# Kernel tuning notes

Hardware: AMD Instinct MI355X
Metric: run time of the kernel (lower is better)

## Reference

```python
import jax, jax.numpy as jnp
import numpy as np

EPS = 1e-5

def _ste(x, q):
    # straight-through estimator: forward=q, backward=identity
    return x + jax.lax.stop_gradient(q - x)

def act_quant(x):
    # per-token int8 absmax quantization (BitNet b1.58 style), fake-quantized
    scale = 127.0 / jnp.clip(jnp.max(jnp.abs(x), axis=-1, keepdims=True), EPS)
    q = jnp.clip(jnp.round(x * scale), -128.0, 127.0) / scale
    return _ste(x, q)

def weight_quant(w):
    # ternary {-1,0,1} weights scaled by mean absolute value
    s = jnp.clip(jnp.mean(jnp.abs(w)), EPS)
    q = jnp.clip(jnp.round(w / s), -1.0, 1.0) * s
    return _ste(w, q)

def bit_linear(x, w):
    # x: [..., in], w: [out, in]
    return jnp.einsum('bsi,oi->bso', act_quant(x), weight_quant(w))

def setup_inputs() -> dict:
    key = jax.random.key(0)
    k1, k2, k3 = jax.random.split(key, 3)
    d_model, hidden = 2048, 4 * 2048
    x = jax.random.normal(k1, (4, 2048, d_model), dtype=jnp.float32)
    w1 = jax.random.normal(k2, (hidden, d_model), dtype=jnp.float32) * 0.02
    w2 = jax.random.normal(k3, (d_model, hidden), dtype=jnp.float32) * 0.02
    return {"x": x, "w1": w1, "w2": w2}

def reference(x, w1, w2):
    h = bit_linear(x, w1)            # [B, S, 4*d]
    h = jax.nn.gelu(h, approximate=False)  # exact erf GELU (nn.GELU default)
    return bit_linear(h, w2)         # [B, S, d]
```

## Files before the change

kernel.cpp:

```cpp
#include <hip/hip_runtime.h>
#include <hip/hip_bf16.h>
#include <hip/hip_fp16.h>
#include <stdint.h>

#define TPB 256
#define EPSF 1e-5f

using i32x4 = __attribute__((ext_vector_type(4))) int;


__device__ __forceinline__ void gload16(const void* g, void* l) {
    __builtin_amdgcn_global_load_lds(
        (__attribute__((address_space(1))) void*)g,
        (__attribute__((address_space(3))) void*)l,
        16, 0, 0);
}

__device__ __forceinline__ float wave_reduce_sum(float v) {
#pragma unroll
    for (int off = 32; off > 0; off >>= 1) v += __shfl_down(v, off, 64);
    return v;
}

__device__ __forceinline__ float wave_reduce_max(float v) {
#pragma unroll
    for (int off = 32; off > 0; off >>= 1) v = fmaxf(v, __shfl_down(v, off, 64));
    return v;
}

__device__ __forceinline__ int q8(float f, float scale, float lo, float hi) {
    return (int)fminf(fmaxf(rintf(f * scale), lo), hi);
}


__global__ void abssum_partial(const float* __restrict__ w, int n4,
                               float* __restrict__ part) {
    const float4* w4 = (const float4*)w;
    float acc = 0.f;
    for (int i = blockIdx.x * TPB + threadIdx.x; i < n4; i += gridDim.x * TPB) {
        float4 v = w4[i];
        acc += fabsf(v.x) + fabsf(v.y) + fabsf(v.z) + fabsf(v.w);
    }
    acc = wave_reduce_sum(acc);
    __shared__ float sh[4];
    if ((threadIdx.x & 63) == 0) sh[threadIdx.x >> 6] = acc;
    __syncthreads();
    if (threadIdx.x == 0) part[blockIdx.x] = sh[0] + sh[1] + sh[2] + sh[3];
}

__global__ void finalize_scales(const float* __restrict__ part1,
                                const float* __restrict__ part2,
                                float* __restrict__ scales, int nparts, float inv_n) {
    float a = 0.f, b = 0.f;
    for (int i = threadIdx.x; i < nparts; i += TPB) { a += part1[i]; b += part2[i]; }
    a = wave_reduce_sum(a);
    b = wave_reduce_sum(b);
    __shared__ float sa[4], sb[4];
    if ((threadIdx.x & 63) == 0) { sa[threadIdx.x >> 6] = a; sb[threadIdx.x >> 6] = b; }
    __syncthreads();
    if (threadIdx.x == 0) {
        scales[0] = fmaxf((sa[0] + sa[1] + sa[2] + sa[3]) * inv_n, EPSF);
        scales[1] = fmaxf((sb[0] + sb[1] + sb[2] + sb[3]) * inv_n, EPSF);
    }
}


__global__ void quant_w_i8(const float* __restrict__ w,
                           signed char* __restrict__ wq,
                           const float* __restrict__ scales, int sidx, int n4) {
    const float inv = 1.0f / scales[sidx];
    const float4* w4 = (const float4*)w;
    unsigned* oq = (unsigned*)wq;
    for (int i = blockIdx.x * TPB + threadIdx.x; i < n4; i += gridDim.x * TPB) {
        float4 v = w4[i];
        unsigned p = ((unsigned)(q8(v.x, inv, -1.f, 1.f) & 0xff)) |
                     ((unsigned)(q8(v.y, inv, -1.f, 1.f) & 0xff) << 8) |
                     ((unsigned)(q8(v.z, inv, -1.f, 1.f) & 0xff) << 16) |
                     ((unsigned)(q8(v.w, inv, -1.f, 1.f) & 0xff) << 24);
        oq[i] = p;
    }
}


template <int NF4>
__global__ void quant_x_i8(const float* __restrict__ in,
                           signed char* __restrict__ outq,
                           float* __restrict__ dq, int cols) {
    const long long row = blockIdx.x;
    const float4* r4 = (const float4*)(in + row * (long long)cols);
    float4 v[NF4];
    float mx = 0.f;
#pragma unroll
    for (int j = 0; j < NF4; ++j) {
        v[j] = r4[threadIdx.x + TPB * j];
        mx = fmaxf(mx, fmaxf(fmaxf(fabsf(v[j].x), fabsf(v[j].y)),
                             fmaxf(fabsf(v[j].z), fabsf(v[j].w))));
    }
    mx = wave_reduce_max(mx);
    __shared__ float sh[4];
    __shared__ float res;
    if ((threadIdx.x & 63) == 0) sh[threadIdx.x >> 6] = mx;
    __syncthreads();
    if (threadIdx.x == 0) res = fmaxf(fmaxf(sh[0], sh[1]), fmaxf(sh[2], sh[3]));
    __syncthreads();
    const float clipped = fmaxf(res, EPSF);
    const float scale = 127.f / clipped;
    if (threadIdx.x == 0) dq[row] = clipped / 127.f;
    unsigned* oq = (unsigned*)(outq + row * (long long)cols);
#pragma unroll
    for (int j = 0; j < NF4; ++j) {
        unsigned p = ((unsigned)(q8(v[j].x, scale, -128.f, 127.f) & 0xff)) |
                     ((unsigned)(q8(v[j].y, scale, -128.f, 127.f) & 0xff) << 8) |
                     ((unsigned)(q8(v[j].z, scale, -128.f, 127.f) & 0xff) << 16) |
                     ((unsigned)(q8(v[j].w, scale, -128.f, 127.f) & 0xff) << 24);
        oq[threadIdx.x + TPB * j] = p;
    }
}


template <int NJ>
__global__ void quant_h_i8(const unsigned short* __restrict__ h,
                           signed char* __restrict__ outq,
                           float* __restrict__ dq, int cols) {
    const long long row = blockIdx.x;
    const unsigned short* rp = h + row * (long long)cols;
    uint4 v[NJ];
    float mx = 0.f;
#pragma unroll
    for (int j = 0; j < NJ; ++j) {
        v[j] = *(const uint4*)(rp + (threadIdx.x + TPB * j) * 8);
        const unsigned* u = (const unsigned*)&v[j];
#pragma unroll
        for (int e = 0; e < 4; ++e) {
            float2 f2 = __half22float2(*(const __half2*)&u[e]);
            mx = fmaxf(mx, fmaxf(fabsf(f2.x), fabsf(f2.y)));
        }
    }
    mx = wave_reduce_max(mx);
    __shared__ float sh[4];
    __shared__ float res;
    if ((threadIdx.x & 63) == 0) sh[threadIdx.x >> 6] = mx;
    __syncthreads();
    if (threadIdx.x == 0) res = fmaxf(fmaxf(sh[0], sh[1]), fmaxf(sh[2], sh[3]));
    __syncthreads();
    const float clipped = fmaxf(res, EPSF);
    const float scale = 127.f / clipped;
    if (threadIdx.x == 0) dq[row] = clipped / 127.f;
    uint2* oq = (uint2*)(outq + row * (long long)cols);
#pragma unroll
    for (int j = 0; j < NJ; ++j) {
        const unsigned* u = (const unsigned*)&v[j];
        unsigned o[2] = {0, 0};
#pragma unroll
        for (int e = 0; e < 4; ++e) {
            float2 f2 = __half22float2(*(const __half2*)&u[e]);
            unsigned b0 = (unsigned)(q8(f2.x, scale, -128.f, 127.f) & 0xff);
            unsigned b1 = (unsigned)(q8(f2.y, scale, -128.f, 127.f) & 0xff);
            o[e >> 1] |= (b0 | (b1 << 8)) << ((e & 1) * 16);
        }
        oq[threadIdx.x + TPB * j] = *(uint2*)o;
    }
}


__device__ __forceinline__ void stage_half(const char* Xb, long long rowB, int prow,
                                           int tk, char* dst, int tid, int cbs) {
    const long long gc = (long long)tk * 128 + cbs;
    const int r = tid >> 3;
    gload16(Xb + (long long)(prow + r) * rowB + gc, dst + tid * 16);
    gload16(Xb + (long long)(prow + 64 + r) * rowB + gc, dst + 8192 + tid * 16);
}

#define QUAD(MB, NB)                                                            \
    _Pragma("unroll") for (int mi = 0; mi < 4; ++mi)                            \
    _Pragma("unroll") for (int ni = 0; ni < 2; ++ni)                            \
    _Pragma("unroll") for (int ks = 0; ks < 2; ++ks)                            \
        acc[(MB)*4 + mi][(NB)*2 + ni] = __builtin_amdgcn_mfma_i32_16x16x64_i8(  \
            aq[mi][ks], bq[(NB)*2 + ni][ks], acc[(MB)*4 + mi][(NB)*2 + ni], 0, 0, 0);

template <int OUT>
__global__ __launch_bounds__(512, 2) void gemm8p_i8(
    const signed char* __restrict__ A, const signed char* __restrict__ B,
    void* __restrict__ Cv, int N, int K,
    const float* __restrict__ dq, const float* __restrict__ scales, int sidx) {
    __shared__ __align__(16) char lds[131072];

    const int tid = threadIdx.x;
    const int lane = tid & 63;
    const int wid = tid >> 6;
    const int wr = wid >> 2;
    const int wc = wid & 3;

    const unsigned gx = gridDim.x;
    unsigned lin = blockIdx.y * gx + blockIdx.x;
    const unsigned qq = (gx * gridDim.y) >> 3;
    lin = (lin & 7) * qq + (lin >> 3);
    const unsigned bx = lin % gx;
    const unsigned by = lin / gx;

    const long long M0 = (long long)by * 256;
    const long long N0 = (long long)bx * 256;
    const long long rb = (long long)K;
    const char* Ab = (const char*)A + M0 * rb;
    const char* Bb = (const char*)B + N0 * rb;
    const int nt = K >> 7;

    const int cbs = (((tid & 7) ^ ((tid >> 3) & 7)) << 4);

    const int l15 = lane & 15, l4 = lane >> 4;
    const int swz = (lane & 7) << 4;
    const int acb0 = (l4 * 16) ^ swz;
    const int acb1 = (64 + l4 * 16) ^ swz;
    const int aoff = wr * 16384;
    const int boff = 32768 + (wc >> 1) * 16384 + (wc & 1) * 8192;

    i32x4 acc[8][4] = {};
    i32x4 aq[4][2], bq[4][2];

    stage_half(Bb, rb, 0,   0, lds + 32768,         tid, cbs);
    stage_half(Bb, rb, 128, 0, lds + 32768 + 16384, tid, cbs);
    stage_half(Ab, rb, 0,   0, lds + 0,             tid, cbs);
    stage_half(Ab, rb, 128, 0, lds + 16384,         tid, cbs);
    if (nt > 1) {
        stage_half(Bb, rb, 0,   1, lds + 65536 + 32768,         tid, cbs);
        stage_half(Bb, rb, 128, 1, lds + 65536 + 32768 + 16384, tid, cbs);
        stage_half(Ab, rb, 0,   1, lds + 65536,                 tid, cbs);
        asm volatile("s_waitcnt vmcnt(6)" ::: "memory");
    } else {
        asm volatile("s_waitcnt vmcnt(0)" ::: "memory");
    }
    __builtin_amdgcn_sched_barrier(0);
    __builtin_amdgcn_s_barrier();

    for (int t = 0; t < nt; ++t) {
        char* cur = lds + ((t & 1) << 16);
        char* nxt = lds + (((t + 1) & 1) << 16);
        const bool s1 = (t + 1) < nt;
        const bool s2 = (t + 2) < nt;

#pragma unroll
        for (int mi = 0; mi < 4; ++mi) {
            const char* p = cur + aoff + (mi * 16 + l15) * 128;
            aq[mi][0] = *(const i32x4*)(p + acb0);
            aq[mi][1] = *(const i32x4*)(p + acb1);
        }
#pragma unroll
        for (int ni = 0; ni < 4; ++ni) {
            const char* p = cur + boff + (ni * 16 + l15) * 128;
            bq[ni][0] = *(const i32x4*)(p + acb0);
            bq[ni][1] = *(const i32x4*)(p + acb1);
        }
        if (s1) stage_half(Ab, rb, 128, t + 1, nxt + 16384, tid, cbs);
        __builtin_amdgcn_s_setprio(1);
        QUAD(0, 0);
        __builtin_amdgcn_s_setprio(0);
        __builtin_amdgcn_s_barrier();

        if (s2) stage_half(Bb, rb, 0, t + 2, cur + 32768, tid, cbs);
        __builtin_amdgcn_s_setprio(1);
        QUAD(0, 1);
        __builtin_amdgcn_s_setprio(0);
        __builtin_amdgcn_s_barrier();

#pragma unroll
        for (int mi = 0; mi < 4; ++mi) {
            const char* p = cur + aoff + ((mi + 4) * 16 + l15) * 128;
            aq[mi][0] = *(const i32x4*)(p + acb0);
            aq[mi][1] = *(const i32x4*)(p + acb1);
        }
        if (s2) stage_half(Bb, rb, 128, t + 2, cur + 32768 + 16384, tid, cbs);
        __builtin_amdgcn_s_setprio(1);
        QUAD(1, 0);
        __builtin_amdgcn_s_setprio(0);
        __builtin_amdgcn_s_barrier();

        if (s2) stage_half(Ab, rb, 0, t + 2, cur, tid, cbs);
        __builtin_amdgcn_s_setprio(1);
        QUAD(1, 1);
        __builtin_amdgcn_s_setprio(0);
        if (s2) { asm volatile("s_waitcnt vmcnt(6)" ::: "memory"); }
        else    { asm volatile("s_waitcnt vmcnt(0)" ::: "memory"); }
        __builtin_amdgcn_sched_barrier(0);
        __builtin_amdgcn_s_barrier();
    }

    const float s = scales[sidx];
#pragma unroll
    for (int mi = 0; mi < 8; ++mi) {
#pragma unroll
        for (int r = 0; r < 4; ++r) {
            const long long m = M0 + wr * 128 + mi * 16 + l4 * 4 + r;
            const float f = dq[m] * s;
#pragma unroll
            for (int ni = 0; ni < 4; ++ni) {
                const long long n = N0 + wc * 64 + ni * 16 + l15;
                float v = (float)acc[mi][ni][r] * f;
                if (OUT) {
                    v = 0.5f * v * (1.0f + erff(v * 0.70710678118654752440f));
                    __half hh = __float2half(v);
                    __builtin_nontemporal_store(
                        *(const unsigned short*)&hh,
                        (unsigned short*)Cv + m * (long long)N + n);
                } else {
                    __builtin_nontemporal_store(
                        v, (float*)Cv + m * (long long)N + n);
                }
            }
        }
    }
}


extern "C" void kernel_launch(void* const* d_in, const int* in_sizes, int n_in,
                              void* d_out, int out_size, void* d_ws, size_t ws_size,
                              hipStream_t stream) {
    (void)n_in; (void)out_size;
    const float* x  = (const float*)d_in[0];
    const float* w1 = (const float*)d_in[1];
    const float* w2 = (const float*)d_in[2];
    float* out = (float*)d_out;

    const int D = 2048, H = 8192;
    const long long M = (long long)in_sizes[0] / D;

    char* base = (char*)d_ws;
    size_t off = 0;
    auto alloc = [&](size_t bytes) -> char* {
        char* r = base + off;
        off = (off + bytes + 255) & ~(size_t)255;
        return r;
    };

    const bool fullM = ws_size >= (size_t)236 * 1024 * 1024;
    const long long MC = fullM ? M : M / 2;

    float* part1 = (float*)alloc(2048 * 4);
    float* part2 = (float*)alloc(2048 * 4);
    float* scales = (float*)alloc(256);
    float* dqx = (float*)alloc((size_t)M * 4);
    float* dqh = (float*)alloc((size_t)M * 4);
    signed char* wq = (signed char*)alloc((size_t)H * D);
    signed char* xq = (signed char*)alloc((size_t)M * D);
    signed char* hq = (signed char*)alloc((size_t)M * H);
    unsigned short* hf = (unsigned short*)alloc((size_t)MC * H * 2);

    const int nw4 = H * D / 4;
    abssum_partial<<<2048, TPB, 0, stream>>>(w1, nw4, part1);
    abssum_partial<<<2048, TPB, 0, stream>>>(w2, nw4, part2);
    finalize_scales<<<1, TPB, 0, stream>>>(part1, part2, scales, 2048,
                                           1.0f / (float)(H * D));
    quant_w_i8<<<2048, TPB, 0, stream>>>(w1, wq, scales, 0, nw4);
    quant_x_i8<2><<<(int)M, TPB, 0, stream>>>(x, xq, dqx, D);

    if (fullM) {
        gemm8p_i8<1><<<dim3(H / 256, (int)(M / 256)), 512, 0, stream>>>(
            xq, wq, hf, H, D, dqx, scales, 0);
        quant_h_i8<4><<<(int)M, TPB, 0, stream>>>(hf, hq, dqh, H);
    } else {
        for (int g = 0; g < 2; ++g) {
            const long long m0 = g * MC;
            gemm8p_i8<1><<<dim3(H / 256, (int)(MC / 256)), 512, 0, stream>>>(
                xq + m0 * D, wq, hf, H, D, dqx + m0, scales, 0);
            quant_h_i8<4><<<(int)MC, TPB, 0, stream>>>(hf, hq + m0 * H, dqh + m0, H);
        }
    }

    quant_w_i8<<<2048, TPB, 0, stream>>>(w2, wq, scales, 1, nw4);

    gemm8p_i8<0><<<dim3(D / 256, (int)(M / 256)), 512, 0, stream>>>(
        hq, wq, out, D, H, dqh, scales, 1);
}
```

Baseline: 408.1 us.

## Switch int8 GEMM to 4-wave 256x128 tiles, fuse abssum, use tanh GELU

The int8 GEMM now runs 256-thread blocks of four waves on 256x128 output tiles instead of 512-thread 256x256 tiles, with a smaller 48KB LDS double buffer. It also changes the XCD-aware block remapping and adds explicit lgkmcnt waits before the MFMA blocks. The two weight abs-sum kernels are merged into one launch. Exact erf GELU is replaced with a tanh-style approximation built on exp2 and rcp, and the fp16 hidden store is no longer nontemporal. The GELU approximation changes numerics slightly, and the smaller tile re-reads the A operand more often in exchange for more blocks per CU.

```diff
diff --git a/kernel.cpp b/kernel.cpp
--- a/kernel.cpp
+++ b/kernel.cpp
@@ -32,12 +32,21 @@
     return (int)fminf(fmaxf(rintf(f * scale), lo), hi);
 }
 
-
-__global__ void abssum_partial(const float* __restrict__ w, int n4,
-                               float* __restrict__ part) {
-    const float4* w4 = (const float4*)w;
+__device__ __forceinline__ float gelu_fast(float x) {
+    float x2 = x * x;
+    float u = x * (0.7978845608f + 0.0356774081f * x2);
+    float e = exp2f(u * -2.8853900817779268f);
+    return x * __builtin_amdgcn_rcpf(1.0f + e);
+}
+
+
+__global__ void abssum2(const float* __restrict__ w1, const float* __restrict__ w2,
+                        int n4, float* __restrict__ part) {
+    const bool second = blockIdx.x >= 2048;
+    const float4* w4 = (const float4*)(second ? w2 : w1);
+    const int b = blockIdx.x & 2047;
     float acc = 0.f;
-    for (int i = blockIdx.x * TPB + threadIdx.x; i < n4; i += gridDim.x * TPB) {
+    for (int i = b * TPB + threadIdx.x; i < n4; i += 2048 * TPB) {
         float4 v = w4[i];
         acc += fabsf(v.x) + fabsf(v.y) + fabsf(v.z) + fabsf(v.w);
     }
@@ -48,11 +57,10 @@
     if (threadIdx.x == 0) part[blockIdx.x] = sh[0] + sh[1] + sh[2] + sh[3];
 }
 
-__global__ void finalize_scales(const float* __restrict__ part1,
-                                const float* __restrict__ part2,
-                                float* __restrict__ scales, int nparts, float inv_n) {
+__global__ void finalize_scales(const float* __restrict__ part,
+                                float* __restrict__ scales, float inv_n) {
     float a = 0.f, b = 0.f;
-    for (int i = threadIdx.x; i < nparts; i += TPB) { a += part1[i]; b += part2[i]; }
+    for (int i = threadIdx.x; i < 2048; i += TPB) { a += part[i]; b += part[i + 2048]; }
     a = wave_reduce_sum(a);
     b = wave_reduce_sum(b);
     __shared__ float sa[4], sb[4];
@@ -163,12 +171,15 @@
 }
 
 
-__device__ __forceinline__ void stage_half(const char* Xb, long long rowB, int prow,
-                                           int tk, char* dst, int tid, int cbs) {
+template <int N32>
+__device__ __forceinline__ void stageN(const char* Xb, long long rowB, int prow,
+                                       int tk, char* dst, int tid, int cbs) {
     const long long gc = (long long)tk * 128 + cbs;
     const int r = tid >> 3;
-    gload16(Xb + (long long)(prow + r) * rowB + gc, dst + tid * 16);
-    gload16(Xb + (long long)(prow + 64 + r) * rowB + gc, dst + 8192 + tid * 16);
+#pragma unroll
+    for (int j = 0; j < N32; ++j)
+        gload16(Xb + (long long)(prow + j * 32 + r) * rowB + gc,
+                dst + j * 4096 + tid * 16);
 }
 
 #define QUAD(MB, NB)                                                            \
@@ -178,54 +189,69 @@
         acc[(MB)*4 + mi][(NB)*2 + ni] = __builtin_amdgcn_mfma_i32_16x16x64_i8(  \
             aq[mi][ks], bq[(NB)*2 + ni][ks], acc[(MB)*4 + mi][(NB)*2 + ni], 0, 0, 0);
 
+#define READ_A(BUF, base_mi)                                                    \
+    _Pragma("unroll") for (int mi = 0; mi < 4; ++mi) {                          \
+        const char* p = (BUF) + aoff + ((mi + (base_mi)) * 16 + l15) * 128;     \
+        aq[mi][0] = *(const i32x4*)(p + acb0);                                  \
+        aq[mi][1] = *(const i32x4*)(p + acb1);                                  \
+    }
+#define READ_B(BUF)                                                             \
+    _Pragma("unroll") for (int ni = 0; ni < 4; ++ni) {                          \
+        const char* p = (BUF) + boff + (ni * 16 + l15) * 128;                   \
+        bq[ni][0] = *(const i32x4*)(p + acb0);                                  \
+        bq[ni][1] = *(const i32x4*)(p + acb1);                                  \
+    }
+
+#define LGKM0 do { asm volatile("s_waitcnt lgkmcnt(0)" ::: "memory");           \
+                   __builtin_amdgcn_sched_barrier(0); } while (0)
+
+#define BUFSZ 49152
+
 template <int OUT>
-__global__ __launch_bounds__(512, 2) void gemm8p_i8(
+__global__ __launch_bounds__(256, 2) void gemm4w(
     const signed char* __restrict__ A, const signed char* __restrict__ B,
     void* __restrict__ Cv, int N, int K,
     const float* __restrict__ dq, const float* __restrict__ scales, int sidx) {
-    __shared__ __align__(16) char lds[131072];
+    __shared__ __align__(16) char lds[2 * BUFSZ];
 
     const int tid = threadIdx.x;
     const int lane = tid & 63;
     const int wid = tid >> 6;
-    const int wr = wid >> 2;
-    const int wc = wid & 3;
+    const int wr = wid >> 1;
+    const int wc = wid & 1;
 
     const unsigned gx = gridDim.x;
-    unsigned lin = blockIdx.y * gx + blockIdx.x;
-    const unsigned qq = (gx * gridDim.y) >> 3;
-    lin = (lin & 7) * qq + (lin >> 3);
-    const unsigned bx = lin % gx;
-    const unsigned by = lin / gx;
+    const unsigned orig = blockIdx.y * gx + blockIdx.x;
+    const unsigned bpx = gx >> 3;
+    const unsigned xcd = orig & 7, jj = orig >> 3;
+    const unsigned bx = xcd * bpx + jj % bpx;
+    const unsigned by = jj / bpx;
 
     const long long M0 = (long long)by * 256;
-    const long long N0 = (long long)bx * 256;
+    const long long N0 = (long long)bx * 128;
     const long long rb = (long long)K;
     const char* Ab = (const char*)A + M0 * rb;
     const char* Bb = (const char*)B + N0 * rb;
     const int nt = K >> 7;
 
     const int cbs = (((tid & 7) ^ ((tid >> 3) & 7)) << 4);
-
     const int l15 = lane & 15, l4 = lane >> 4;
     const int swz = (lane & 7) << 4;
     const int acb0 = (l4 * 16) ^ swz;
     const int acb1 = (64 + l4 * 16) ^ swz;
     const int aoff = wr * 16384;
-    const int boff = 32768 + (wc >> 1) * 16384 + (wc & 1) * 8192;
+    const int boff = 32768 + wc * 8192;
 
     i32x4 acc[8][4] = {};
     i32x4 aq[4][2], bq[4][2];
 
-    stage_half(Bb, rb, 0,   0, lds + 32768,         tid, cbs);
-    stage_half(Bb, rb, 128, 0, lds + 32768 + 16384, tid, cbs);
-    stage_half(Ab, rb, 0,   0, lds + 0,             tid, cbs);
-    stage_half(Ab, rb, 128, 0, lds + 16384,         tid, cbs);
+    stageN<4>(Bb, rb, 0,   0, lds + 32768, tid, cbs);
+    stageN<4>(Ab, rb, 0,   0, lds + 0,     tid, cbs);
+    stageN<4>(Ab, rb, 128, 0, lds + 16384, tid, cbs);
     if (nt > 1) {
-        stage_half(Bb, rb, 0,   1, lds + 65536 + 32768,         tid, cbs);
-        stage_half(Bb, rb, 128, 1, lds + 65536 + 32768 + 16384, tid, cbs);
-        stage_half(Ab, rb, 0,   1, lds + 65536,                 tid, cbs);
-        asm volatile("s_waitcnt vmcnt(6)" ::: "memory");
+        stageN<4>(Bb, rb, 0, 1, lds + BUFSZ + 32768, tid, cbs);
+        stageN<4>(Ab, rb, 0, 1, lds + BUFSZ,         tid, cbs);
+        asm volatile("s_waitcnt vmcnt(8)" ::: "memory");
     } else {
         asm volatile("s_waitcnt vmcnt(0)" ::: "memory");
     }
@@ -233,52 +259,39 @@
     __builtin_amdgcn_s_barrier();
 
     for (int t = 0; t < nt; ++t) {
-        char* cur = lds + ((t & 1) << 16);
-        char* nxt = lds + (((t + 1) & 1) << 16);
+        char* cur = lds + (t & 1) * BUFSZ;
+        char* nxt = lds + ((t + 1) & 1) * BUFSZ;
         const bool s1 = (t + 1) < nt;
         const bool s2 = (t + 2) < nt;
 
-#pragma unroll
-        for (int mi = 0; mi < 4; ++mi) {
-            const char* p = cur + aoff + (mi * 16 + l15) * 128;
-            aq[mi][0] = *(const i32x4*)(p + acb0);
-            aq[mi][1] = *(const i32x4*)(p + acb1);
-        }
-#pragma unroll
-        for (int ni = 0; ni < 4; ++ni) {
-            const char* p = cur + boff + (ni * 16 + l15) * 128;
-            bq[ni][0] = *(const i32x4*)(p + acb0);
-            bq[ni][1] = *(const i32x4*)(p + acb1);
-        }
-        if (s1) stage_half(Ab, rb, 128, t + 1, nxt + 16384, tid, cbs);
+        READ_A(cur, 0);
+        READ_B(cur);
+        if (s1) stageN<4>(Ab, rb, 128, t + 1, nxt + 16384, tid, cbs);
+        LGKM0;
         __builtin_amdgcn_s_setprio(1);
         QUAD(0, 0);
         __builtin_amdgcn_s_setprio(0);
         __builtin_amdgcn_s_barrier();
 
-        if (s2) stage_half(Bb, rb, 0, t + 2, cur + 32768, tid, cbs);
+        if (s2) stageN<2>(Bb, rb, 0, t + 2, cur + 32768, tid, cbs);
         __builtin_amdgcn_s_setprio(1);
         QUAD(0, 1);
         __builtin_amdgcn_s_setprio(0);
         __builtin_amdgcn_s_barrier();
 
-#pragma unroll
-        for (int mi = 0; mi < 4; ++mi) {
-            const char* p = cur + aoff + ((mi + 4) * 16 + l15) * 128;
-            aq[mi][0] = *(const i32x4*)(p + acb0);
-            aq[mi][1] = *(const i32x4*)(p + acb1);
-        }
-        if (s2) stage_half(Bb, rb, 128, t + 2, cur + 32768 + 16384, tid, cbs);
+        READ_A(cur, 4);
+        if (s2) stageN<2>(Bb, rb, 64, t + 2, cur + 40960, tid, cbs);
+        LGKM0;
         __builtin_amdgcn_s_setprio(1);
         QUAD(1, 0);
         __builtin_amdgcn_s_setprio(0);
         __builtin_amdgcn_s_barrier();
 
-        if (s2) stage_half(Ab, rb, 0, t + 2, cur, tid, cbs);
+        if (s2) stageN<4>(Ab, rb, 0, t + 2, cur, tid, cbs);
         __builtin_amdgcn_s_setprio(1);
         QUAD(1, 1);
         __builtin_amdgcn_s_setprio(0);
-        if (s2) { asm volatile("s_waitcnt vmcnt(6)" ::: "memory"); }
+        if (s2) { asm volatile("s_waitcnt vmcnt(8)" ::: "memory"); }
         else    { asm volatile("s_waitcnt vmcnt(0)" ::: "memory"); }
         __builtin_amdgcn_sched_barrier(0);
         __builtin_amdgcn_s_barrier();
@@ -296,11 +309,10 @@
                 const long long n = N0 + wc * 64 + ni * 16 + l15;
                 float v = (float)acc[mi][ni][r] * f;
                 if (OUT) {
-                    v = 0.5f * v * (1.0f + erff(v * 0.70710678118654752440f));
+                    v = gelu_fast(v);
                     __half hh = __float2half(v);
-                    __builtin_nontemporal_store(
-                        *(const unsigned short*)&hh,
-                        (unsigned short*)Cv + m * (long long)N + n);
+                    ((unsigned short*)Cv)[m * (long long)N + n] =
+                        *(const unsigned short*)&hh;
                 } else {
                     __builtin_nontemporal_store(
                         v, (float*)Cv + m * (long long)N + n);
@@ -334,8 +346,7 @@
     const bool fullM = ws_size >= (size_t)236 * 1024 * 1024;
     const long long MC = fullM ? M : M / 2;
 
-    float* part1 = (float*)alloc(2048 * 4);
-    float* part2 = (float*)alloc(2048 * 4);
+    float* part = (float*)alloc(4096 * 4);
     float* scales = (float*)alloc(256);
     float* dqx = (float*)alloc((size_t)M * 4);
     float* dqh = (float*)alloc((size_t)M * 4);
@@ -345,21 +356,19 @@
     unsigned short* hf = (unsigned short*)alloc((size_t)MC * H * 2);
 
     const int nw4 = H * D / 4;
-    abssum_partial<<<2048, TPB, 0, stream>>>(w1, nw4, part1);
-    abssum_partial<<<2048, TPB, 0, stream>>>(w2, nw4, part2);
-    finalize_scales<<<1, TPB, 0, stream>>>(part1, part2, scales, 2048,
-                                           1.0f / (float)(H * D));
+    abssum2<<<4096, TPB, 0, stream>>>(w1, w2, nw4, part);
+    finalize_scales<<<1, TPB, 0, stream>>>(part, scales, 1.0f / (float)(H * D));
     quant_w_i8<<<2048, TPB, 0, stream>>>(w1, wq, scales, 0, nw4);
     quant_x_i8<2><<<(int)M, TPB, 0, stream>>>(x, xq, dqx, D);
 
     if (fullM) {
-        gemm8p_i8<1><<<dim3(H / 256, (int)(M / 256)), 512, 0, stream>>>(
+        gemm4w<1><<<dim3(H / 128, (int)(M / 256)), 256, 0, stream>>>(
             xq, wq, hf, H, D, dqx, scales, 0);
         quant_h_i8<4><<<(int)M, TPB, 0, stream>>>(hf, hq, dqh, H);
     } else {
         for (int g = 0; g < 2; ++g) {
             const long long m0 = g * MC;
-            gemm8p_i8<1><<<dim3(H / 256, (int)(MC / 256)), 512, 0, stream>>>(
+            gemm4w<1><<<dim3(H / 128, (int)(MC / 256)), 256, 0, stream>>>(
                 xq + m0 * D, wq, hf, H, D, dqx + m0, scales, 0);
             quant_h_i8<4><<<(int)MC, TPB, 0, stream>>>(hf, hq + m0 * H, dqh + m0, H);
         }
@@ -367,6 +376,6 @@
 
     quant_w_i8<<<2048, TPB, 0, stream>>>(w2, wq, scales, 1, nw4);
 
-    gemm8p_i8<0><<<dim3(D / 256, (int)(M / 256)), 512, 0, stream>>>(
+    gemm4w<0><<<dim3(D / 128, (int)(M / 256)), 256, 0, stream>>>(
         hq, wq, out, D, H, dqh, scales, 1);
 }
```

New measurement: 431.1 us. 1.06x slower.
